# Kernel optimization log

Hardware: AMD Instinct MI355X
Metric: run time of the kernel (lower is better)

The kernel has to match this reference:

```python
import jax, jax.numpy as jnp
import numpy as np

D_MODEL = 1024
N_HEADS = 16
D_K = D_MODEL // N_HEADS
ROPE_BASE = 10000.0


def _rope_cos_sin(seq_len, dim):
    # matches calc_rope_theta: freqs over even indices of head dim
    freqs = jnp.arange(0, dim, 2, dtype=jnp.float32) / dim
    inv_freq = 1.0 / (ROPE_BASE ** freqs)                      # [dim/2]
    pos = jnp.arange(seq_len, dtype=jnp.float32)               # [S]
    ang = pos[:, None] * inv_freq[None, :]                     # [S, dim/2]
    return jnp.cos(ang), jnp.sin(ang)


def _apply_rope(x, cos, sin):
    # x: [N, S, dk]; complex pairs are consecutive elements (view_as_complex)
    x0 = x[..., 0::2]
    x1 = x[..., 1::2]
    r = x0 * cos - x1 * sin
    i = x0 * sin + x1 * cos
    return jnp.stack([r, i], axis=-1).reshape(x.shape)


def setup_inputs() -> dict:
    key = jax.random.key(0)
    ks = jax.random.split(key, 11)
    B, S, D = 4, 1024, D_MODEL
    w = lambda k: jax.random.normal(k, (D, D), dtype=jnp.float32) * 0.02
    b = lambda k: jax.random.normal(k, (D,), dtype=jnp.float32) * 0.02
    return {
        "q": jax.random.normal(ks[0], (B, S, D), dtype=jnp.float32),
        "k": jax.random.normal(ks[1], (B, S, D), dtype=jnp.float32),
        "v": jax.random.normal(ks[2], (B, S, D), dtype=jnp.float32),
        "Wq": w(ks[3]), "bq": b(ks[4]),
        "Wk": w(ks[5]), "bk": b(ks[6]),
        "Wv": w(ks[7]), "bv": b(ks[8]),
        "Wo": w(ks[9]), "bo": b(ks[10]),
    }


def reference(q, k, v, Wq, bq, Wk, bk, Wv, bv, Wo, bo):
    B, S, D = q.shape
    H, dk = N_HEADS, D_K
    qp = (q @ Wq + bq).reshape(B, S, H, dk)
    kp = (k @ Wk + bk).reshape(B, S, H, dk)
    vp = (v @ Wv + bv).reshape(B, S, H, dk)

    cos, sin = _rope_cos_sin(S, dk)
    # Faithful to source: raw reshape (B,S,H,dk)->(-1,S,dk) before RoPE
    qp = _apply_rope(qp.reshape(-1, S, dk), cos, sin).reshape(B, S, H, dk)
    kp = _apply_rope(kp.reshape(-1, S, dk), cos, sin).reshape(B, S, H, dk)

    qh = qp.transpose(0, 2, 1, 3)  # [B,H,S,dk]
    kh = kp.transpose(0, 2, 1, 3)
    vh = vp.transpose(0, 2, 1, 3)

    scores = jnp.einsum("bhqd,bhkd->bhqk", qh, kh) / jnp.sqrt(jnp.float32(dk))
    attn = jax.nn.softmax(scores, axis=-1)
    out = jnp.einsum("bhqk,bhkd->bhqd", attn, vh)
    out = out.transpose(0, 2, 1, 3).reshape(B, S, D)
    return out @ Wo + bo
```

## Files before the change

kernel.cpp:

```cpp
#include <hip/hip_runtime.h>

typedef __attribute__((ext_vector_type(8))) short bf16x8;
typedef __attribute__((ext_vector_type(4))) short short4v;
typedef __attribute__((ext_vector_type(4))) float f32x4;

#define MFMA16x16x32(a, b, c) __builtin_amdgcn_mfma_f32_16x16x32_bf16((a), (b), (c), 0, 0, 0)

__device__ __forceinline__ short f2bf(float f) {
    unsigned u = __builtin_bit_cast(unsigned, f);
    u += 0x7FFFu + ((u >> 16) & 1u);
    return (short)(u >> 16);
}

__device__ __forceinline__ void gl_lds16(const void* g, void* l) {
    __builtin_amdgcn_global_load_lds((__attribute__((address_space(1))) void*)g,
                                     (__attribute__((address_space(3))) void*)l,
                                     16, 0, 0);
}

__device__ __forceinline__ void cvt16(const float* __restrict__ p, bf16x8& lo, bf16x8& hi) {
    f32x4 a = *(const f32x4*)(p);
    f32x4 b = *(const f32x4*)(p + 4);
    f32x4 c = *(const f32x4*)(p + 8);
    f32x4 d = *(const f32x4*)(p + 12);
#pragma unroll
    for (int i = 0; i < 4; ++i) {
        lo[i]     = f2bf(a[i]);
        lo[i + 4] = f2bf(b[i]);
        hi[i]     = f2bf(c[i]);
        hi[i + 4] = f2bf(d[i]);
    }
}

__global__ __launch_bounds__(256) void cvt3(const float* __restrict__ x0,
                                            const float* __restrict__ x1,
                                            const float* __restrict__ x2,
                                            short* __restrict__ y) {
    int sel = blockIdx.y;
    const float* x = sel == 0 ? x0 : (sel == 1 ? x1 : x2);
    short* yy = y + (size_t)sel * (1 << 22);
    int i = (blockIdx.x * 256 + threadIdx.x) * 16;
    bf16x8 lo, hi;
    cvt16(x + i, lo, hi);
    *(bf16x8*)(yy + i)     = lo;
    *(bf16x8*)(yy + i + 8) = hi;
}

__global__ __launch_bounds__(256) void transW4(const float* __restrict__ w0,
                                               const float* __restrict__ w1,
                                               const float* __restrict__ w2,
                                               const float* __restrict__ w3,
                                               short* __restrict__ wt) {
    __shared__ short t[64][80];
    int z = blockIdx.z;
    const float* W = z == 0 ? w0 : (z == 1 ? w1 : (z == 2 ? w2 : w3));
    short* Wt = wt + (size_t)z * (1 << 20);
    int bx = blockIdx.x, by = blockIdx.y;
    int tid = threadIdx.x;
    int sr = tid >> 2, sc = (tid & 3) * 16;
    bf16x8 lo, hi;
    cvt16(W + (by * 64 + sr) * 1024 + bx * 64 + sc, lo, hi);
    *(bf16x8*)&t[sr][sc]     = lo;
    *(bf16x8*)&t[sr][sc + 8] = hi;
    __syncthreads();
    bf16x8 o0, o1;
#pragma unroll
    for (int i = 0; i < 8; ++i) {
        o0[i] = t[sc + i][sr];
        o1[i] = t[sc + 8 + i][sr];
    }
    short* dst = Wt + (bx * 64 + sr) * 1024 + by * 64 + sc;
    *(bf16x8*)(dst)     = o0;
    *(bf16x8*)(dst + 8) = o1;
}

template <int MODE>
__global__ __launch_bounds__(256) void gemm_nt(const short* __restrict__ A,
                                               const short* __restrict__ Bt,
                                               const float* __restrict__ bias,
                                               void* __restrict__ dstv) {
    __shared__ short As[2][128 * 64];
    __shared__ short Bs[2][64 * 64];
    const int K = 1024;
    int tid = threadIdx.x;
    int bn = blockIdx.x, bm = blockIdx.y;
    int wave = tid >> 6, lane = tid & 63;
    int quad = lane >> 4, l16 = lane & 15;
    int wm = (wave >> 1) * 64, wn = (wave & 1) * 32;

    f32x4 acc[4][2] = {};

    auto stage = [&](int b, int kb) {
#pragma unroll
        for (int j = 0; j < 4; ++j) {
            int c = j * 256 + tid;
            gl_lds16(A + (bm * 128 + (c >> 3)) * K + kb + (c & 7) * 8, &As[b][c * 8]);
        }
#pragma unroll
        for (int j = 0; j < 2; ++j) {
            int c = j * 256 + tid;
            gl_lds16(Bt + (bn * 64 + (c >> 3)) * K + kb + (c & 7) * 8, &Bs[b][c * 8]);
        }
    };

    stage(0, 0);
    __syncthreads();

    for (int kb = 0; kb < K; kb += 64) {
        int cur = (kb >> 6) & 1;
        if (kb + 64 < K) stage(cur ^ 1, kb + 64);
#pragma unroll
        for (int ks = 0; ks < 2; ++ks) {
            bf16x8 bf0 = *(const bf16x8*)&Bs[cur][(wn + l16) * 64 + ks * 32 + quad * 8];
            bf16x8 bf1 = *(const bf16x8*)&Bs[cur][(wn + 16 + l16) * 64 + ks * 32 + quad * 8];
#pragma unroll
            for (int mi = 0; mi < 4; ++mi) {
                bf16x8 af = *(const bf16x8*)&As[cur][(wm + mi * 16 + l16) * 64 + ks * 32 + quad * 8];
                acc[mi][0] = MFMA16x16x32(af, bf0, acc[mi][0]);
                acc[mi][1] = MFMA16x16x32(af, bf1, acc[mi][1]);
            }
        }
        __syncthreads();
    }

    int row0 = bm * 128 + wm;
    int col0 = bn * 64 + wn;
#pragma unroll
    for (int mi = 0; mi < 4; ++mi) {
#pragma unroll
        for (int ni = 0; ni < 2; ++ni) {
            int gn = col0 + ni * 16 + l16;
            float bv = bias[gn];
            f32x4 c = acc[mi][ni];
            if constexpr (MODE == 0) {
                short* dst = (short*)dstv;
                int h = gn >> 6, dd = gn & 63;
                float inv = exp2f(-(float)(dd >> 1) * 0.41524101186092029f);
#pragma unroll
                for (int r = 0; r < 4; ++r) {
                    int gm = row0 + mi * 16 + quad * 4 + r;
                    int s = gm & 1023, b = gm >> 10;
                    int p = ((s << 4) + h) & 1023;
                    float val = c[r] + bv;
                    float partner = __shfl_xor(val, 1);
                    float sn, cs;
                    __sincosf((float)p * inv, &sn, &cs);
                    float res = (dd & 1) ? fmaf(partner, sn, val * cs)
                                         : fmaf(val, cs, -(partner * sn));
                    dst[((b * 16 + h) * 1024 + s) * 64 + dd] = f2bf(res);
                }
            } else if constexpr (MODE == 2) {
                short* dst = (short*)dstv;
                int h = gn >> 6, dd = gn & 63;
                int gm0 = row0 + mi * 16 + quad * 4;
                int s0 = gm0 & 1023, b = gm0 >> 10;
                short4v pack;
#pragma unroll
                for (int r = 0; r < 4; ++r) pack[r] = f2bf(c[r] + bv);
                *(short4v*)&dst[((b * 16 + h) * 64 + dd) * 1024 + s0] = pack;
            } else {
                float* dst = (float*)dstv;
#pragma unroll
                for (int r = 0; r < 4; ++r) {
                    int gm = row0 + mi * 16 + quad * 4 + r;
                    dst[gm * 1024 + gn] = c[r] + bv;
                }
            }
        }
    }
}

__global__ __launch_bounds__(512) void attn_kernel(const short* __restrict__ Qh,
                                                   const short* __restrict__ Kh,
                                                   const short* __restrict__ Vt,
                                                   short* __restrict__ O) {
    __shared__ short Ks[2][32 * 64];
    __shared__ short Vs[2][64 * 32];
    __shared__ short Pl[8][16 * 40];
    int tid = threadIdx.x;
    int wave = tid >> 6, lane = tid & 63;
    int quad = lane >> 4, l16 = lane & 15;
    int bh = blockIdx.x & 63, qt = blockIdx.x >> 6;
    int qrow = qt * 128 + wave * 16;

    const short* Qp = Qh + (bh * 1024 + qrow) * 64;
    bf16x8 aq[2];
#pragma unroll
    for (int kh = 0; kh < 2; ++kh)
        aq[kh] = *(const bf16x8*)&Qp[l16 * 64 + kh * 32 + quad * 8];

    const short* Kp = Kh + bh * 1024 * 64;
    const short* Vp = Vt + bh * 64 * 1024;

    int ck = tid & 255;
    bool isV = tid >= 256;
    int krow = ck >> 3;
    int vrow = ck >> 2;
    int ksrc = krow * 64 + (((ck & 7) ^ (krow & 7)) * 8);
    int vsrc = vrow * 1024 + ((((ck & 3) ^ (vrow & 3) ^ ((vrow >> 2) & 3)) & 3) * 8);

    int ksw  = l16 & 7;
    int vswr = (l16 & 3) ^ ((l16 >> 2) & 3);

    float l_i[4] = {};
    f32x4 oa[4] = {};

    if (!isV) gl_lds16(Kp + ksrc, &Ks[0][ck * 8]);
    else      gl_lds16(Vp + vsrc, &Vs[0][ck * 8]);
    __syncthreads();

    short* Pw = &Pl[wave][0];

    for (int kb = 0; kb < 1024; kb += 32) {
        int cur = (kb >> 5) & 1, nxt = cur ^ 1;
        int kb2 = (kb + 32) & 1023;
        if (!isV) gl_lds16(Kp + kb2 * 64 + ksrc, &Ks[nxt][ck * 8]);
        else      gl_lds16(Vp + kb2 + vsrc,      &Vs[nxt][ck * 8]);

#pragma unroll
        for (int g = 0; g < 2; ++g) {
            f32x4 s = {};
#pragma unroll
            for (int kh = 0; kh < 2; ++kh) {
                bf16x8 bk = *(const bf16x8*)
                    &Ks[cur][(g * 16 + l16) * 64 + (((kh * 4 + quad) ^ ksw) * 8)];
                s = MFMA16x16x32(aq[kh], bk, s);
            }
#pragma unroll
            for (int r = 0; r < 4; ++r) {
                float p = exp2f(s[r] * 0.18033688011112042f);
                l_i[r] += p;
                Pw[(quad * 4 + r) * 40 + g * 16 + l16] = f2bf(p);
            }
        }

        bf16x8 bv[4];
#pragma unroll
        for (int t = 0; t < 4; ++t)
            bv[t] = *(const bf16x8*)&Vs[cur][(t * 16 + l16) * 32 + ((quad ^ vswr) * 8)];

        asm volatile("s_waitcnt lgkmcnt(0)" ::: "memory");
        bf16x8 ap = *(const bf16x8*)&Pw[l16 * 40 + quad * 8];

#pragma unroll
        for (int t = 0; t < 4; ++t)
            oa[t] = MFMA16x16x32(ap, bv[t], oa[t]);

        __syncthreads();
    }

#pragma unroll
    for (int d = 1; d < 16; d <<= 1)
#pragma unroll
        for (int r = 0; r < 4; ++r) l_i[r] += __shfl_xor(l_i[r], d);

    float inv[4];
#pragma unroll
    for (int r = 0; r < 4; ++r) inv[r] = 1.0f / l_i[r];

    int b = bh >> 4, h = bh & 15;
#pragma unroll
    for (int t = 0; t < 4; ++t)
#pragma unroll
        for (int r = 0; r < 4; ++r) {
            int s = qrow + quad * 4 + r;
            O[(b * 1024 + s) * 1024 + h * 64 + t * 16 + l16] = f2bf(oa[t][r] * inv[r]);
        }
}

extern "C" void kernel_launch(void* const* d_in, const int* in_sizes, int n_in,
                              void* d_out, int out_size, void* d_ws, size_t ws_size,
                              hipStream_t stream) {
    const float* q  = (const float*)d_in[0];
    const float* k  = (const float*)d_in[1];
    const float* v  = (const float*)d_in[2];
    const float* Wq = (const float*)d_in[3];
    const float* bq = (const float*)d_in[4];
    const float* Wk = (const float*)d_in[5];
    const float* bk = (const float*)d_in[6];
    const float* Wv = (const float*)d_in[7];
    const float* bv = (const float*)d_in[8];
    const float* Wo = (const float*)d_in[9];
    const float* bo = (const float*)d_in[10];

    short* qb   = (short*)d_ws;
    short* kbuf = qb + (4 << 20);
    short* vb   = kbuf + (4 << 20);
    short* wt   = vb + (4 << 20);
    short* wtq  = wt;
    short* wtk  = wt + (1 << 20);
    short* wtv  = wt + (2 << 20);
    short* wto  = wt + (3 << 20);
    short* vt   = qb;
    short* obuf = kbuf;

    short* qh  = (short*)d_out;
    short* kh  = qh + (4 << 20);
    float* out = (float*)d_out;

    cvt3<<<dim3(1024, 3), 256, 0, stream>>>(q, k, v, qb);
    transW4<<<dim3(16, 16, 4), 256, 0, stream>>>(Wq, Wk, Wv, Wo, wt);

    dim3 ggrid(16, 32);
    gemm_nt<0><<<ggrid, 256, 0, stream>>>(qb,   wtq, bq, qh);
    gemm_nt<0><<<ggrid, 256, 0, stream>>>(kbuf, wtk, bk, kh);
    gemm_nt<2><<<ggrid, 256, 0, stream>>>(vb,   wtv, bv, vt);

    attn_kernel<<<512, 512, 0, stream>>>(qh, kh, vt, obuf);

    gemm_nt<3><<<ggrid, 256, 0, stream>>>(obuf, wto, bo, out);
}
```

Baseline: 242.1 us.

## Widen GEMM tiles to 128x128, batch Q/K projections, and tweak attention inner loop

The projection GEMMs now use 128x128 output tiles with a 4x4 MFMA accumulator per wave. Launches are flattened with XCD-aware block mapping, and the Q and K projections are merged into one launch. In attention, the QK MFMA operands are swapped so each lane holds one key column's scores, which lets P be written with packed bf16 converts as 8-byte stores. The per-row sum reduction shrinks to two shuffles, and s_setprio is raised around the MFMA blocks. The larger tiles should cut LDS and global traffic per FLOP and launch overhead, at the cost of more registers and fewer blocks (256 for the single GEMMs) on a large GPU.

```diff
diff --git a/kernel.cpp b/kernel.cpp
--- a/kernel.cpp
+++ b/kernel.cpp
@@ -3,6 +3,7 @@
 typedef __attribute__((ext_vector_type(8))) short bf16x8;
 typedef __attribute__((ext_vector_type(4))) short short4v;
 typedef __attribute__((ext_vector_type(4))) float f32x4;
+typedef __attribute__((ext_vector_type(2))) unsigned u32x2;
 
 #define MFMA16x16x32(a, b, c) __builtin_amdgcn_mfma_f32_16x16x32_bf16((a), (b), (c), 0, 0, 0)
 
@@ -10,6 +11,12 @@
     unsigned u = __builtin_bit_cast(unsigned, f);
     u += 0x7FFFu + ((u >> 16) & 1u);
     return (short)(u >> 16);
+}
+
+__device__ __forceinline__ unsigned cvtpk(float lo, float hi) {
+    unsigned r;
+    asm("v_cvt_pk_bf16_f32 %0, %1, %2" : "=v"(r) : "v"(lo), "v"(hi));
+    return r;
 }
 
 __device__ __forceinline__ void gl_lds16(const void* g, void* l) {
@@ -74,32 +81,45 @@
     *(bf16x8*)(dst + 8) = o1;
 }
 
-template <int MODE>
-__global__ __launch_bounds__(256) void gemm_nt(const short* __restrict__ A,
-                                               const short* __restrict__ Bt,
-                                               const float* __restrict__ bias,
-                                               void* __restrict__ dstv) {
+template <int MODE, int NZ>
+__global__ __launch_bounds__(256) void gemm128(const short* __restrict__ A0,
+                                               const short* __restrict__ A1,
+                                               const short* __restrict__ Bt0,
+                                               const short* __restrict__ Bt1,
+                                               const float* __restrict__ b0,
+                                               const float* __restrict__ b1,
+                                               void* __restrict__ d0,
+                                               void* __restrict__ d1) {
     __shared__ short As[2][128 * 64];
-    __shared__ short Bs[2][64 * 64];
+    __shared__ short Bs[2][128 * 64];
     const int K = 1024;
+    int flat = blockIdx.x;
+    int xcd = flat & 7, j = flat >> 3;
+    int bm = xcd * 4 + (j & 3);
+    int bn = (j >> 2) & 7;
+    int z  = (NZ == 2) ? (j >> 5) : 0;
+    const short* A    = z ? A1 : A0;
+    const short* Bt   = z ? Bt1 : Bt0;
+    const float* bias = z ? b1 : b0;
+    void* dstv        = z ? d1 : d0;
+
     int tid = threadIdx.x;
-    int bn = blockIdx.x, bm = blockIdx.y;
     int wave = tid >> 6, lane = tid & 63;
     int quad = lane >> 4, l16 = lane & 15;
-    int wm = (wave >> 1) * 64, wn = (wave & 1) * 32;
-
-    f32x4 acc[4][2] = {};
+    int wm = (wave >> 1) * 64, wn = (wave & 1) * 64;
+
+    f32x4 acc[4][4] = {};
 
     auto stage = [&](int b, int kb) {
 #pragma unroll
-        for (int j = 0; j < 4; ++j) {
-            int c = j * 256 + tid;
+        for (int jj = 0; jj < 4; ++jj) {
+            int c = jj * 256 + tid;
             gl_lds16(A + (bm * 128 + (c >> 3)) * K + kb + (c & 7) * 8, &As[b][c * 8]);
         }
 #pragma unroll
-        for (int j = 0; j < 2; ++j) {
-            int c = j * 256 + tid;
-            gl_lds16(Bt + (bn * 64 + (c >> 3)) * K + kb + (c & 7) * 8, &Bs[b][c * 8]);
+        for (int jj = 0; jj < 4; ++jj) {
+            int c = jj * 256 + tid;
+            gl_lds16(Bt + (bn * 128 + (c >> 3)) * K + kb + (c & 7) * 8, &Bs[b][c * 8]);
         }
     };
 
@@ -111,24 +131,27 @@
         if (kb + 64 < K) stage(cur ^ 1, kb + 64);
 #pragma unroll
         for (int ks = 0; ks < 2; ++ks) {
-            bf16x8 bf0 = *(const bf16x8*)&Bs[cur][(wn + l16) * 64 + ks * 32 + quad * 8];
-            bf16x8 bf1 = *(const bf16x8*)&Bs[cur][(wn + 16 + l16) * 64 + ks * 32 + quad * 8];
+            bf16x8 bf[4];
+#pragma unroll
+            for (int ni = 0; ni < 4; ++ni)
+                bf[ni] = *(const bf16x8*)&Bs[cur][(wn + ni * 16 + l16) * 64 + ks * 32 + quad * 8];
 #pragma unroll
             for (int mi = 0; mi < 4; ++mi) {
                 bf16x8 af = *(const bf16x8*)&As[cur][(wm + mi * 16 + l16) * 64 + ks * 32 + quad * 8];
-                acc[mi][0] = MFMA16x16x32(af, bf0, acc[mi][0]);
-                acc[mi][1] = MFMA16x16x32(af, bf1, acc[mi][1]);
+#pragma unroll
+                for (int ni = 0; ni < 4; ++ni)
+                    acc[mi][ni] = MFMA16x16x32(af, bf[ni], acc[mi][ni]);
             }
         }
         __syncthreads();
     }
 
     int row0 = bm * 128 + wm;
-    int col0 = bn * 64 + wn;
+    int col0 = bn * 128 + wn;
 #pragma unroll
     for (int mi = 0; mi < 4; ++mi) {
 #pragma unroll
-        for (int ni = 0; ni < 2; ++ni) {
+        for (int ni = 0; ni < 4; ++ni) {
             int gn = col0 + ni * 16 + l16;
             float bv = bias[gn];
             f32x4 c = acc[mi][ni];
@@ -202,7 +225,7 @@
     int ksw  = l16 & 7;
     int vswr = (l16 & 3) ^ ((l16 >> 2) & 3);
 
-    float l_i[4] = {};
+    float lsum = 0.f;
     f32x4 oa[4] = {};
 
     if (!isV) gl_lds16(Kp + ksrc, &Ks[0][ck * 8]);
@@ -220,18 +243,24 @@
 #pragma unroll
         for (int g = 0; g < 2; ++g) {
             f32x4 s = {};
+            __builtin_amdgcn_s_setprio(1);
 #pragma unroll
             for (int kh = 0; kh < 2; ++kh) {
-                bf16x8 bk = *(const bf16x8*)
+                bf16x8 ak = *(const bf16x8*)
                     &Ks[cur][(g * 16 + l16) * 64 + (((kh * 4 + quad) ^ ksw) * 8)];
-                s = MFMA16x16x32(aq[kh], bk, s);
+                s = MFMA16x16x32(ak, aq[kh], s);
             }
+            __builtin_amdgcn_s_setprio(0);
+            float p[4];
 #pragma unroll
             for (int r = 0; r < 4; ++r) {
-                float p = exp2f(s[r] * 0.18033688011112042f);
-                l_i[r] += p;
-                Pw[(quad * 4 + r) * 40 + g * 16 + l16] = f2bf(p);
+                p[r] = exp2f(s[r] * 0.18033688011112042f);
+                lsum += p[r];
             }
+            u32x2 w;
+            w[0] = cvtpk(p[0], p[1]);
+            w[1] = cvtpk(p[2], p[3]);
+            *(u32x2*)&Pw[l16 * 40 + g * 16 + quad * 4] = w;
         }
 
         bf16x8 bv[4];
@@ -242,21 +271,21 @@
         asm volatile("s_waitcnt lgkmcnt(0)" ::: "memory");
         bf16x8 ap = *(const bf16x8*)&Pw[l16 * 40 + quad * 8];
 
+        __builtin_amdgcn_s_setprio(1);
 #pragma unroll
         for (int t = 0; t < 4; ++t)
             oa[t] = MFMA16x16x32(ap, bv[t], oa[t]);
+        __builtin_amdgcn_s_setprio(0);
 
         __syncthreads();
     }
 
-#pragma unroll
-    for (int d = 1; d < 16; d <<= 1)
-#pragma unroll
-        for (int r = 0; r < 4; ++r) l_i[r] += __shfl_xor(l_i[r], d);
-
+    lsum += __shfl_xor(lsum, 16);
+    lsum += __shfl_xor(lsum, 32);
     float inv[4];
 #pragma unroll
-    for (int r = 0; r < 4; ++r) inv[r] = 1.0f / l_i[r];
+    for (int r = 0; r < 4; ++r)
+        inv[r] = 1.0f / __shfl(lsum, (lane & 48) + ((lane >> 4) & 3) * 4 + r);
 
     int b = bh >> 4, h = bh & 15;
 #pragma unroll
@@ -301,12 +330,10 @@
     cvt3<<<dim3(1024, 3), 256, 0, stream>>>(q, k, v, qb);
     transW4<<<dim3(16, 16, 4), 256, 0, stream>>>(Wq, Wk, Wv, Wo, wt);
 
-    dim3 ggrid(16, 32);
-    gemm_nt<0><<<ggrid, 256, 0, stream>>>(qb,   wtq, bq, qh);
-    gemm_nt<0><<<ggrid, 256, 0, stream>>>(kbuf, wtk, bk, kh);
-    gemm_nt<2><<<ggrid, 256, 0, stream>>>(vb,   wtv, bv, vt);
+    gemm128<0, 2><<<512, 256, 0, stream>>>(qb, kbuf, wtq, wtk, bq, bk, qh, kh);
+    gemm128<2, 1><<<256, 256, 0, stream>>>(vb, vb, wtv, wtv, bv, bv, vt, vt);
 
     attn_kernel<<<512, 512, 0, stream>>>(qh, kh, vt, obuf);
 
-    gemm_nt<3><<<ggrid, 256, 0, stream>>>(obuf, wto, bo, out);
-}
+    gemm128<3, 1><<<256, 256, 0, stream>>>(obuf, obuf, wto, wto, bo, bo, out, out);
+}
```

Measured after the change: 223.3 us. 7.8% less time.
